# Kernel tuning notes

Measured on AMD Instinct MI355X. Metric: run time of the kernel, lower is better.

## Reference

```python
import jax, jax.numpy as jnp
import numpy as np

B, S, E, H, D, P = 4, 2048, 1024, 16, 64, 64  # batch, seq, embed, heads, head_dim, position_dim
MASKED_BIAS = -10000.0


def setup_inputs() -> dict:
    key = jax.random.key(0)
    ks = jax.random.split(key, 24)
    n = lambda k, sh: jax.random.normal(k, sh, dtype=jnp.float32)
    eyeD = jnp.eye(D, dtype=jnp.float32)
    eyeH = jnp.eye(H, dtype=jnp.float32)
    inp = {
        'hidden_states': n(ks[0], (B, S, E)),
        'position_states': n(ks[1], (B, S, P)),
        # Conv2D per-head projections (identity init + perturbation): [H, D, D]
        'Wq': eyeD[None] + 0.02 * n(ks[2], (H, D, D)), 'bq': 0.01 * n(ks[3], (H, D)),
        'Wk': eyeD[None] + 0.02 * n(ks[4], (H, D, D)), 'bk': 0.01 * n(ks[5], (H, D)),
        'Wv': eyeD[None] + 0.02 * n(ks[6], (H, D, D)), 'bv': 0.01 * n(ks[7], (H, D)),
        # Conv2D(transpose=True) cross-head mix: weight [H_out, H_in, D], bias [H, D]
        'Wqh': eyeH[:, :, None] + 0.02 * n(ks[8], (H, H, D)), 'bqh': 0.01 * n(ks[9], (H, D)),
        'Wkh': eyeH[:, :, None] + 0.02 * n(ks[10], (H, H, D)), 'bkh': 0.01 * n(ks[11], (H, D)),
        'Wvh': eyeH[:, :, None] + 0.02 * n(ks[12], (H, H, D)), 'bvh': 0.01 * n(ks[13], (H, D)),
        # p_attn Conv1D: position_dim -> 3*head_dim
        'Wp': 0.02 * n(ks[14], (P, 3 * D)), 'bp': 0.01 * n(ks[15], (3 * D,)),
        # position_conv expand: weight [3, 1, H], bias [H]
        'Wpe': 0.02 * n(ks[16], (3, 1, H)), 'bpe': 0.01 * n(ks[17], (H,)),
        # c_proj Conv1D: E -> E
        'Wc': 0.02 * n(ks[18], (E, E)), 'bc': 0.01 * n(ks[19], (E,)),
    }
    return inp


def _attention(hidden_states, position_states, Wq, bq, Wqh, bqh, Wk, bk, Wkh, bkh,
               Wv, bv, Wvh, bvh, Wp, bp, Wpe, bpe, Wc, bc):
    b, s, _ = hidden_states.shape
    x = hidden_states.reshape(b, s, H, D)

    def proj(Wa, ba, Wh, bh):
        # Conv2D: per-head linear within head_dim
        y = jnp.einsum('bshd,hde->bshe', x, Wa) + ba
        # Conv2D(transpose): mix across heads, per feature dim d
        return jnp.einsum('bshd,ghd->bsgd', y, Wh) + bh

    q = proj(Wq, bq, Wqh, bqh)  # [b,s,H,D]
    k = proj(Wk, bk, Wkh, bkh)
    v = proj(Wv, bv, Wvh, bvh)

    # p_attn (Conv1D) -> [b,s,3,D]; p_expand broadcasts each var across heads
    p = (position_states @ Wp + bp).reshape(b, s, 3, D)
    pe = p[..., None, :] * Wpe[:, 0, :][:, :, None] + bpe[:, None]  # [b,s,3,H,D]
    q = q + pe[:, :, 0]
    k = k + pe[:, :, 1]
    v = v + pe[:, :, 2]

    q = q.transpose(0, 2, 1, 3)  # [b,H,s,D]
    k = k.transpose(0, 2, 1, 3)
    v = v.transpose(0, 2, 1, 3)

    scores = jnp.einsum('bhqd,bhkd->bhqk', q, k) / jnp.sqrt(jnp.float32(D))
    causal = jnp.tril(jnp.ones((s, s), dtype=bool))
    scores = jnp.where(causal, scores, jnp.float32(MASKED_BIAS))
    w = jax.nn.softmax(scores, axis=-1)
    o = jnp.einsum('bhqk,bhkd->bhqd', w, v)
    o = o.transpose(0, 2, 1, 3).reshape(b, s, E)
    return o @ Wc + bc


def reference(hidden_states, position_states, Wq, bq, Wqh, bqh, Wk, bk, Wkh, bkh,
              Wv, bv, Wvh, bvh, Wp, bp, Wpe, bpe, Wc, bc):
    return _attention(hidden_states, position_states, Wq, bq, Wqh, bqh, Wk, bk,
                      Wkh, bkh, Wv, bv, Wvh, bvh, Wp, bp, Wpe, bpe, Wc, bc)
```

## Files before the change

kernel.cpp:

```cpp
#include <hip/hip_runtime.h>
#include <stdint.h>
#include <stddef.h>

using bf16x8 = __attribute__((ext_vector_type(8))) __bf16;
using f32x4  = __attribute__((ext_vector_type(4))) float;
using u16x8  = __attribute__((ext_vector_type(8))) unsigned short;
using u16x4  = __attribute__((ext_vector_type(4))) unsigned short;
typedef unsigned short u16;

#define DEV __device__ __forceinline__

#define QSCALE 0.18033688011112042f
#define SBIAS 32.0f

DEV u16 f2bf(float f) {
  unsigned u = __float_as_uint(f);
  u += 0x7fffu + ((u >> 16) & 1u);
  return (u16)(u >> 16);
}

DEV void gld_lds16(const u16* g, u16* l) {
  __builtin_amdgcn_global_load_lds(
      (__attribute__((address_space(1))) void*)g,
      (__attribute__((address_space(3))) void*)l, 16, 0, 0);
}

__global__ __launch_bounds__(256) void k_packA(const float* __restrict__ hs,
                                               const float* __restrict__ ps,
                                               u16* __restrict__ A) {
  int idx = blockIdx.x * 256 + threadIdx.x;
  int t  = idx / 272;
  int c4 = (idx - t * 272) * 4;
  float4 f;
  if (c4 < 1024) f = *(const float4*)(hs + (size_t)t * 1024 + c4);
  else           f = *(const float4*)(ps + (size_t)t * 64 + (c4 - 1024));
  u16x4 o4;
  o4[0] = f2bf(f.x); o4[1] = f2bf(f.y); o4[2] = f2bf(f.z); o4[3] = f2bf(f.w);
  *(u16x4*)(A + (size_t)t * 1088 + c4) = o4;
}

__global__ __launch_bounds__(256) void k_buildW(const float* __restrict__ Wq, const float* __restrict__ Wk,
                                                const float* __restrict__ Wv, const float* __restrict__ Wqh,
                                                const float* __restrict__ Wkh, const float* __restrict__ Wvh,
                                                const float* __restrict__ Wp, const float* __restrict__ Wpe,
                                                u16* __restrict__ Wt) {
  int idx = blockIdx.x * 256 + threadIdx.x;
  int n = idx / 1088, kk = idx - n * 1088;
  int which = n >> 10, g = (n >> 6) & 15, e = n & 63;
  const float* Wa = (which == 0) ? Wq : (which == 1) ? Wk : Wv;
  const float* Wh = (which == 0) ? Wqh : (which == 1) ? Wkh : Wvh;
  float val;
  if (kk < 1024) {
    int h = kk >> 6, d = kk & 63;
    val = Wa[(size_t)(h * 64 + d) * 64 + e] * Wh[(size_t)(g * 16 + h) * 64 + e];
  } else {
    int p = kk - 1024;
    val = Wp[(size_t)p * 192 + which * 64 + e] * Wpe[which * 16 + g];
  }
  if (which == 0) val *= QSCALE;
  Wt[idx] = f2bf(val);
}

__global__ __launch_bounds__(256) void k_buildBias(const float* __restrict__ bq, const float* __restrict__ bk,
                                                   const float* __restrict__ bv, const float* __restrict__ Wqh,
                                                   const float* __restrict__ Wkh, const float* __restrict__ Wvh,
                                                   const float* __restrict__ bqh, const float* __restrict__ bkh,
                                                   const float* __restrict__ bvh, const float* __restrict__ bp,
                                                   const float* __restrict__ Wpe, const float* __restrict__ bpe,
                                                   float* __restrict__ bias) {
  int n = blockIdx.x * 256 + threadIdx.x;
  int which = n >> 10, g = (n >> 6) & 15, e = n & 63;
  const float* ba = (which == 0) ? bq : (which == 1) ? bk : bv;
  const float* Wh = (which == 0) ? Wqh : (which == 1) ? Wkh : Wvh;
  const float* bh = (which == 0) ? bqh : (which == 1) ? bkh : bvh;
  float s = bh[g * 64 + e] + bp[which * 64 + e] * Wpe[which * 16 + g] + bpe[g];
  for (int h = 0; h < 16; ++h) s += ba[h * 64 + e] * Wh[(g * 16 + h) * 64 + e];
  if (which == 0) s *= QSCALE;
  bias[n] = s;
}

__global__ __launch_bounds__(256) void k_transWc(const float* __restrict__ Wc, u16* __restrict__ WcT) {
  __shared__ float tile[32][33];
  int tx = threadIdx.x & 31, ty = threadIdx.x >> 5;
  int n0 = blockIdx.x * 32, k0 = blockIdx.y * 32;
#pragma unroll
  for (int i = 0; i < 32; i += 8)
    tile[ty + i][tx] = Wc[(size_t)(k0 + ty + i) * 1024 + n0 + tx];
  __syncthreads();
#pragma unroll
  for (int i = 0; i < 32; i += 8)
    WcT[(size_t)(n0 + ty + i) * 1024 + k0 + tx] = f2bf(tile[tx][ty + i]);
}

template <int EPI>
__global__ __launch_bounds__(256) void gemm128(const u16* __restrict__ A, const u16* __restrict__ Bt,
                                               const float* __restrict__ bias,
                                               u16* __restrict__ qo, u16* __restrict__ ko, u16* __restrict__ vo,
                                               float* __restrict__ outf, int M, int N, int K, int NT) {
  __shared__ alignas(16) u16 As[2][8192];
  __shared__ alignas(16) u16 Bs[2][8192];
  const int tid = threadIdx.x;
  const int l = tid & 63, w = tid >> 6;
  const int lr = l & 15, lg = l >> 4;
  const int wm = w >> 1, wn = w & 1;

  const int nwg = gridDim.x;
  const int cpx = nwg >> 3;
  const int virt = (blockIdx.x & 7) * cpx + (blockIdx.x >> 3);
  const int m0 = (virt / NT) * 128, n0 = (virt - (virt / NT) * NT) * 128;

  const int KT = K >> 6;

  f32x4 acc[4][4] = {};

#pragma unroll
  for (int call = 0; call < 4; ++call) {
    int ci = (call * 4 + w) * 64 + l;
    int row = ci >> 3, s = ci & 7;
    int kq = (s ^ (row & 7)) * 8;
    gld_lds16(A + (size_t)(m0 + row) * K + kq, &As[0][(call * 4 + w) * 512]);
    gld_lds16(Bt + (size_t)(n0 + row) * K + kq, &Bs[0][(call * 4 + w) * 512]);
  }

  int cur = 0;
  for (int kt = 0; kt < KT; ++kt) {
    if (kt + 1 < KT) {
      const int kb = (kt + 1) * 64;
#pragma unroll
      for (int call = 0; call < 4; ++call) {
        int ci = (call * 4 + w) * 64 + l;
        int row = ci >> 3, s = ci & 7;
        int kq = (s ^ (row & 7)) * 8;
        gld_lds16(A + (size_t)(m0 + row) * K + kb + kq, &As[cur ^ 1][(call * 4 + w) * 512]);
        gld_lds16(Bt + (size_t)(n0 + row) * K + kb + kq, &Bs[cur ^ 1][(call * 4 + w) * 512]);
      }
      asm volatile("s_waitcnt vmcnt(8)" ::: "memory");
    } else {
      asm volatile("s_waitcnt vmcnt(0)" ::: "memory");
    }
    __builtin_amdgcn_s_barrier();
    asm volatile("" ::: "memory");

    const u16* AsC = As[cur];
    const u16* BsC = Bs[cur];
#pragma unroll
    for (int kk = 0; kk < 2; ++kk) {
      bf16x8 af[4], bfr[4];
#pragma unroll
      for (int mf = 0; mf < 4; ++mf) {
        int row = wm * 64 + mf * 16 + lr;
        int byo = row * 128 + (((kk * 32 + lg * 8) * 2) ^ ((row & 7) << 4));
        af[mf] = *(const bf16x8*)((const char*)AsC + byo);
      }
#pragma unroll
      for (int nf = 0; nf < 4; ++nf) {
        int row = wn * 64 + nf * 16 + lr;
        int byo = row * 128 + (((kk * 32 + lg * 8) * 2) ^ ((row & 7) << 4));
        bfr[nf] = *(const bf16x8*)((const char*)BsC + byo);
      }
      __builtin_amdgcn_s_setprio(1);
#pragma unroll
      for (int mf = 0; mf < 4; ++mf)
#pragma unroll
        for (int nf = 0; nf < 4; ++nf)
          acc[mf][nf] = __builtin_amdgcn_mfma_f32_16x16x32_bf16(af[mf], bfr[nf], acc[mf][nf], 0, 0, 0);
      __builtin_amdgcn_s_setprio(0);
    }

    asm volatile("s_waitcnt lgkmcnt(0)" ::: "memory");
    __builtin_amdgcn_s_barrier();
    asm volatile("" ::: "memory");
    cur ^= 1;
  }

#pragma unroll
  for (int mf = 0; mf < 4; ++mf)
#pragma unroll
    for (int nf = 0; nf < 4; ++nf)
#pragma unroll
      for (int r = 0; r < 4; ++r) {
        int row = m0 + wm * 64 + mf * 16 + lg * 4 + r;
        int col = n0 + wn * 64 + nf * 16 + lr;
        float val = acc[mf][nf][r] + bias[col];
        if (EPI == 0) {
          int which = col >> 10, g = (col >> 6) & 15, e = col & 63;
          int b = row >> 11, si = row & 2047;
          size_t idx = ((size_t)((b * 16 + g) * 2048 + si)) * 64 + e;
          u16 bvv = f2bf(val);
          if (which == 0) qo[idx] = bvv;
          else if (which == 1) ko[idx] = bvv;
          else vo[idx] = bvv;
        } else {
          outf[(size_t)row * N + col] = val;
        }
      }
}

__global__ __launch_bounds__(256) void k_transV(const u16* __restrict__ v, u16* __restrict__ vT) {
  __shared__ u16 t[64][65];
  int bh = blockIdx.y, s0 = blockIdx.x * 64;
  const u16* src = v + ((size_t)bh * 2048 + s0) * 64;
  u16* dst = vT + (size_t)bh * 64 * 2048 + s0;
  int tid = threadIdx.x;
#pragma unroll
  for (int it = 0; it < 2; ++it) {
    int ci = it * 256 + tid;
    int row = ci >> 3, sl = ci & 7;
    u16x8 val = *(const u16x8*)(src + (size_t)row * 64 + sl * 8);
#pragma unroll
    for (int jj = 0; jj < 8; ++jj) t[row][sl * 8 + jj] = val[jj];
  }
  __syncthreads();
#pragma unroll
  for (int it = 0; it < 2; ++it) {
    int ci = it * 256 + tid;
    int d = ci >> 3, sl = ci & 7;
    u16x8 val;
#pragma unroll
    for (int jj = 0; jj < 8; ++jj) {
      int cp = sl * 8 + jj;
      int tt = (cp & 3) * 16 + (cp >> 2);
      val[jj] = t[tt][d];
    }
    *(u16x8*)(dst + (size_t)d * 2048 + sl * 8) = val;
  }
}

__global__ __launch_bounds__(512) void k_attn(const u16* __restrict__ q, const u16* __restrict__ k,
                                              const u16* __restrict__ vt, u16* __restrict__ o) {
  __shared__ alignas(16) u16 Ks[2][4096];
  __shared__ alignas(16) u16 Vs[2][4096];
  __shared__ alignas(16) u16 Ps[8][16 * 72];

  const int tid = threadIdx.x, l = tid & 63, w = tid >> 6;
  const int lr = l & 15, lg = l >> 4;
  const int i = blockIdx.x;
  const int bh = (i & 7) * 8 + ((i >> 3) & 7);
  const int xb = i >> 6;
  const int b = bh >> 4, h = bh & 15;

  const u16* qp = q + (size_t)bh * 2048 * 64;
  const u16* kp = k + (size_t)bh * 2048 * 64;
  const u16* vp = vt + (size_t)bh * 64 * 2048;

  const int srow = tid >> 3;
  const int skq = ((tid & 7) ^ (srow & 7)) * 8;

  bf16x8 ones;
#pragma unroll
  for (int e = 0; e < 8; ++e) ones[e] = (__bf16)1.0f;

  for (int half = 0; half < 2; ++half) {
    const int tile = half ? (15 - xb) : xb;
    const int qr0 = tile * 128 + w * 16;
    const int jmax = 2 * tile + 1;
    const int jmask = qr0 >> 6;

    bf16x8 qf[2];
#pragma unroll
    for (int kk = 0; kk < 2; ++kk)
      qf[kk] = *(const bf16x8*)(qp + (size_t)(qr0 + lr) * 64 + kk * 32 + lg * 8);

    f32x4 oacc[4] = {};
    f32x4 osum = {};

    gld_lds16(kp + (size_t)srow * 64 + skq, &Ks[0][w * 512]);
    gld_lds16(vp + (size_t)srow * 2048 + skq, &Vs[0][w * 512]);

    int cur = 0;
    for (int j = 0; j <= jmax; ++j) {
      if (j < jmax) {
        const int jn = j + 1;
        gld_lds16(kp + (size_t)(jn * 64 + srow) * 64 + skq, &Ks[cur ^ 1][w * 512]);
        gld_lds16(vp + (size_t)srow * 2048 + jn * 64 + skq, &Vs[cur ^ 1][w * 512]);
        asm volatile("s_waitcnt vmcnt(2)" ::: "memory");
      } else {
        asm volatile("s_waitcnt vmcnt(0)" ::: "memory");
      }
      __builtin_amdgcn_s_barrier();
      asm volatile("" ::: "memory");

      if (j <= jmask) {
        const u16* KsC = Ks[cur];
        const u16* VsC = Vs[cur];

        f32x4 sfr[4];
#pragma unroll
        for (int nf = 0; nf < 4; ++nf)
          sfr[nf] = f32x4{-SBIAS, -SBIAS, -SBIAS, -SBIAS};
#pragma unroll
        for (int kk = 0; kk < 2; ++kk) {
          bf16x8 bk[4];
#pragma unroll
          for (int nf = 0; nf < 4; ++nf) {
            int row = nf * 16 + lr;
            int byo = row * 128 + (((kk * 32 + lg * 8) * 2) ^ ((row & 7) << 4));
            bk[nf] = *(const bf16x8*)((const char*)KsC + byo);
          }
          __builtin_amdgcn_s_setprio(1);
#pragma unroll
          for (int nf = 0; nf < 4; ++nf)
            sfr[nf] = __builtin_amdgcn_mfma_f32_16x16x32_bf16(qf[kk], bk[nf], sfr[nf], 0, 0, 0);
          __builtin_amdgcn_s_setprio(0);
        }

        const bool maskt = (j == jmask);
#pragma unroll
        for (int r = 0; r < 4; ++r) {
          float s0 = sfr[0][r], s1 = sfr[1][r], s2 = sfr[2][r], s3 = sfr[3][r];
          if (maskt) {
            int rowg = qr0 + lg * 4 + r;
            int base = j * 64 + lr;
            if (base      > rowg) s0 = -1e30f;
            if (base + 16 > rowg) s1 = -1e30f;
            if (base + 32 > rowg) s2 = -1e30f;
            if (base + 48 > rowg) s3 = -1e30f;
          }
          float p0 = __builtin_amdgcn_exp2f(s0);
          float p1 = __builtin_amdgcn_exp2f(s1);
          float p2 = __builtin_amdgcn_exp2f(s2);
          float p3 = __builtin_amdgcn_exp2f(s3);
          unsigned w0, w1;
          asm("v_cvt_pk_bf16_f32 %0, %1, %2" : "=v"(w0) : "v"(p0), "v"(p1));
          asm("v_cvt_pk_bf16_f32 %0, %1, %2" : "=v"(w1) : "v"(p2), "v"(p3));
          uint2 pw; pw.x = w0; pw.y = w1;
          *(uint2*)&Ps[w][(lg * 4 + r) * 72 + 4 * lr] = pw;
        }

#pragma unroll
        for (int kk = 0; kk < 2; ++kk) {
          bf16x8 pa = *(const bf16x8*)&Ps[w][lr * 72 + kk * 32 + lg * 8];
          bf16x8 bv[4];
#pragma unroll
          for (int df = 0; df < 4; ++df) {
            int row = df * 16 + lr;
            int byo = row * 128 + (((kk * 32 + lg * 8) * 2) ^ ((row & 7) << 4));
            bv[df] = *(const bf16x8*)((const char*)VsC + byo);
          }
          __builtin_amdgcn_s_setprio(1);
#pragma unroll
          for (int df = 0; df < 4; ++df)
            oacc[df] = __builtin_amdgcn_mfma_f32_16x16x32_bf16(pa, bv[df], oacc[df], 0, 0, 0);
          osum = __builtin_amdgcn_mfma_f32_16x16x32_bf16(pa, ones, osum, 0, 0, 0);
          __builtin_amdgcn_s_setprio(0);
        }
      }

      asm volatile("s_waitcnt lgkmcnt(0)" ::: "memory");
      __builtin_amdgcn_s_barrier();
      asm volatile("" ::: "memory");
      cur ^= 1;
    }

#pragma unroll
    for (int r = 0; r < 4; ++r) {
      float inv = 1.0f / osum[r];
      int rowg = qr0 + lg * 4 + r;
#pragma unroll
      for (int df = 0; df < 4; ++df)
        o[((size_t)(b * 2048 + rowg)) * 1024 + h * 64 + df * 16 + lr] = f2bf(oacc[df][r] * inv);
    }
  }
}

extern "C" void kernel_launch(void* const* d_in, const int* in_sizes, int n_in,
                              void* d_out, int out_size, void* d_ws, size_t ws_size,
                              hipStream_t stream) {
  const float* hs  = (const float*)d_in[0];
  const float* pos = (const float*)d_in[1];
  const float* Wq  = (const float*)d_in[2];  const float* bq  = (const float*)d_in[3];
  const float* Wk  = (const float*)d_in[4];  const float* bk  = (const float*)d_in[5];
  const float* Wv  = (const float*)d_in[6];  const float* bv  = (const float*)d_in[7];
  const float* Wqh = (const float*)d_in[8];  const float* bqh = (const float*)d_in[9];
  const float* Wkh = (const float*)d_in[10]; const float* bkh = (const float*)d_in[11];
  const float* Wvh = (const float*)d_in[12]; const float* bvh = (const float*)d_in[13];
  const float* Wp  = (const float*)d_in[14]; const float* bp  = (const float*)d_in[15];
  const float* Wpe = (const float*)d_in[16]; const float* bpe = (const float*)d_in[17];
  const float* Wc  = (const float*)d_in[18]; const float* bc  = (const float*)d_in[19];
  float* out = (float*)d_out;
  char* ws = (char*)d_ws;

  u16*   Abf   = (u16*)  (ws + 0);
  u16*   WT    = (u16*)  (ws + 17825792);
  float* biasq = (float*)(ws + 24510464);
  u16*   WcT   = (u16*)  (ws + 24522752);
  u16*   qb_   = (u16*)  (ws + 26619904);
  u16*   kb_   = (u16*)  (ws + 43397120);
  u16*   vb_   = (u16*)  (ws + 60174336);
  u16*   vTb   = (u16*)  (ws + 76951552);
  u16*   ob    = Abf;

  k_packA<<<8704, 256, 0, stream>>>(hs, pos, Abf);
  k_buildW<<<13056, 256, 0, stream>>>(Wq, Wk, Wv, Wqh, Wkh, Wvh, Wp, Wpe, WT);
  k_buildBias<<<12, 256, 0, stream>>>(bq, bk, bv, Wqh, Wkh, Wvh, bqh, bkh, bvh, bp, Wpe, bpe, biasq);
  k_transWc<<<dim3(32, 32), 256, 0, stream>>>(Wc, WcT);
  gemm128<0><<<1536, 256, 0, stream>>>(Abf, WT, biasq, qb_, kb_, vb_, nullptr, 8192, 3072, 1088, 24);
  k_transV<<<dim3(32, 64), 256, 0, stream>>>(vb_, vTb);
  k_attn<<<512, 512, 0, stream>>>(qb_, kb_, vTb, ob);
  gemm128<1><<<512, 256, 0, stream>>>(ob, WcT, bc, nullptr, nullptr, nullptr, out, 8192, 1024, 1024, 8);
}
```

Measured before the change: 179.4 us.

## Process 32 query rows per wave in attention with 4-wave blocks

```diff
diff --git a/kernel.cpp b/kernel.cpp
--- a/kernel.cpp
+++ b/kernel.cpp
@@ -226,11 +226,11 @@
   }
 }
 
-__global__ __launch_bounds__(512) void k_attn(const u16* __restrict__ q, const u16* __restrict__ k,
+__global__ __launch_bounds__(256) void k_attn(const u16* __restrict__ q, const u16* __restrict__ k,
                                               const u16* __restrict__ vt, u16* __restrict__ o) {
   __shared__ alignas(16) u16 Ks[2][4096];
   __shared__ alignas(16) u16 Vs[2][4096];
-  __shared__ alignas(16) u16 Ps[8][16 * 72];
+  __shared__ alignas(16) u16 Ps[4][32 * 72];
 
   const int tid = threadIdx.x, l = tid & 63, w = tid >> 6;
   const int lr = l & 15, lg = l >> 4;
@@ -243,37 +243,48 @@
   const u16* kp = k + (size_t)bh * 2048 * 64;
   const u16* vp = vt + (size_t)bh * 64 * 2048;
 
-  const int srow = tid >> 3;
-  const int skq = ((tid & 7) ^ (srow & 7)) * 8;
-
   bf16x8 ones;
 #pragma unroll
   for (int e = 0; e < 8; ++e) ones[e] = (__bf16)1.0f;
 
   for (int half = 0; half < 2; ++half) {
     const int tile = half ? (15 - xb) : xb;
-    const int qr0 = tile * 128 + w * 16;
+    const int qr0 = tile * 128 + w * 32;
     const int jmax = 2 * tile + 1;
-    const int jmask = qr0 >> 6;
-
-    bf16x8 qf[2];
-#pragma unroll
-    for (int kk = 0; kk < 2; ++kk)
-      qf[kk] = *(const bf16x8*)(qp + (size_t)(qr0 + lr) * 64 + kk * 32 + lg * 8);
-
-    f32x4 oacc[4] = {};
-    f32x4 osum = {};
-
-    gld_lds16(kp + (size_t)srow * 64 + skq, &Ks[0][w * 512]);
-    gld_lds16(vp + (size_t)srow * 2048 + skq, &Vs[0][w * 512]);
+    const int jmask = (qr0 + 31) >> 6;
+
+    bf16x8 qf[2][2];
+#pragma unroll
+    for (int mf = 0; mf < 2; ++mf)
+#pragma unroll
+      for (int kk = 0; kk < 2; ++kk)
+        qf[mf][kk] = *(const bf16x8*)(qp + (size_t)(qr0 + mf * 16 + lr) * 64 + kk * 32 + lg * 8);
+
+    f32x4 oacc[2][4] = {};
+    f32x4 osum[2] = {};
+
+#pragma unroll
+    for (int c = 0; c < 2; ++c) {
+      int ci = c * 256 + tid;
+      int row = ci >> 3, s = ci & 7;
+      int kq = (s ^ (row & 7)) * 8;
+      gld_lds16(kp + (size_t)row * 64 + kq, &Ks[0][(c * 4 + w) * 512]);
+      gld_lds16(vp + (size_t)row * 2048 + kq, &Vs[0][(c * 4 + w) * 512]);
+    }
 
     int cur = 0;
     for (int j = 0; j <= jmax; ++j) {
       if (j < jmax) {
         const int jn = j + 1;
-        gld_lds16(kp + (size_t)(jn * 64 + srow) * 64 + skq, &Ks[cur ^ 1][w * 512]);
-        gld_lds16(vp + (size_t)srow * 2048 + jn * 64 + skq, &Vs[cur ^ 1][w * 512]);
-        asm volatile("s_waitcnt vmcnt(2)" ::: "memory");
+#pragma unroll
+        for (int c = 0; c < 2; ++c) {
+          int ci = c * 256 + tid;
+          int row = ci >> 3, s = ci & 7;
+          int kq = (s ^ (row & 7)) * 8;
+          gld_lds16(kp + (size_t)(jn * 64 + row) * 64 + kq, &Ks[cur ^ 1][(c * 4 + w) * 512]);
+          gld_lds16(vp + (size_t)row * 2048 + jn * 64 + kq, &Vs[cur ^ 1][(c * 4 + w) * 512]);
+        }
+        asm volatile("s_waitcnt vmcnt(4)" ::: "memory");
       } else {
         asm volatile("s_waitcnt vmcnt(0)" ::: "memory");
       }
@@ -284,10 +295,12 @@
         const u16* KsC = Ks[cur];
         const u16* VsC = Vs[cur];
 
-        f32x4 sfr[4];
-#pragma unroll
-        for (int nf = 0; nf < 4; ++nf)
-          sfr[nf] = f32x4{-SBIAS, -SBIAS, -SBIAS, -SBIAS};
+        f32x4 sfr[2][4];
+#pragma unroll
+        for (int mf = 0; mf < 2; ++mf)
+#pragma unroll
+          for (int nf = 0; nf < 4; ++nf)
+            sfr[mf][nf] = f32x4{-SBIAS, -SBIAS, -SBIAS, -SBIAS};
 #pragma unroll
         for (int kk = 0; kk < 2; ++kk) {
           bf16x8 bk[4];
@@ -299,37 +312,44 @@
           }
           __builtin_amdgcn_s_setprio(1);
 #pragma unroll
-          for (int nf = 0; nf < 4; ++nf)
-            sfr[nf] = __builtin_amdgcn_mfma_f32_16x16x32_bf16(qf[kk], bk[nf], sfr[nf], 0, 0, 0);
+          for (int mf = 0; mf < 2; ++mf)
+#pragma unroll
+            for (int nf = 0; nf < 4; ++nf)
+              sfr[mf][nf] = __builtin_amdgcn_mfma_f32_16x16x32_bf16(qf[mf][kk], bk[nf], sfr[mf][nf], 0, 0, 0);
           __builtin_amdgcn_s_setprio(0);
         }
 
         const bool maskt = (j == jmask);
 #pragma unroll
-        for (int r = 0; r < 4; ++r) {
-          float s0 = sfr[0][r], s1 = sfr[1][r], s2 = sfr[2][r], s3 = sfr[3][r];
-          if (maskt) {
-            int rowg = qr0 + lg * 4 + r;
-            int base = j * 64 + lr;
-            if (base      > rowg) s0 = -1e30f;
-            if (base + 16 > rowg) s1 = -1e30f;
-            if (base + 32 > rowg) s2 = -1e30f;
-            if (base + 48 > rowg) s3 = -1e30f;
+        for (int mf = 0; mf < 2; ++mf)
+#pragma unroll
+          for (int r = 0; r < 4; ++r) {
+            float s0 = sfr[mf][0][r], s1 = sfr[mf][1][r], s2 = sfr[mf][2][r], s3 = sfr[mf][3][r];
+            if (maskt) {
+              int rowg = qr0 + mf * 16 + lg * 4 + r;
+              int base = j * 64 + lr;
+              if (base      > rowg) s0 = -1e30f;
+              if (base + 16 > rowg) s1 = -1e30f;
+              if (base + 32 > rowg) s2 = -1e30f;
+              if (base + 48 > rowg) s3 = -1e30f;
+            }
+            float p0 = __builtin_amdgcn_exp2f(s0);
+            float p1 = __builtin_amdgcn_exp2f(s1);
+            float p2 = __builtin_amdgcn_exp2f(s2);
+            float p3 = __builtin_amdgcn_exp2f(s3);
+            unsigned w0, w1;
+            asm("v_cvt_pk_bf16_f32 %0, %1, %2" : "=v"(w0) : "v"(p0), "v"(p1));
+            asm("v_cvt_pk_bf16_f32 %0, %1, %2" : "=v"(w1) : "v"(p2), "v"(p3));
+            uint2 pw; pw.x = w0; pw.y = w1;
+            *(uint2*)&Ps[w][(mf * 16 + lg * 4 + r) * 72 + 4 * lr] = pw;
           }
-          float p0 = __builtin_amdgcn_exp2f(s0);
-          float p1 = __builtin_amdgcn_exp2f(s1);
-          float p2 = __builtin_amdgcn_exp2f(s2);
-          float p3 = __builtin_amdgcn_exp2f(s3);
-          unsigned w0, w1;
-          asm("v_cvt_pk_bf16_f32 %0, %1, %2" : "=v"(w0) : "v"(p0), "v"(p1));
-          asm("v_cvt_pk_bf16_f32 %0, %1, %2" : "=v"(w1) : "v"(p2), "v"(p3));
-          uint2 pw; pw.x = w0; pw.y = w1;
-          *(uint2*)&Ps[w][(lg * 4 + r) * 72 + 4 * lr] = pw;
-        }
 
 #pragma unroll
         for (int kk = 0; kk < 2; ++kk) {
-          bf16x8 pa = *(const bf16x8*)&Ps[w][lr * 72 + kk * 32 + lg * 8];
+          bf16x8 pa[2];
+#pragma unroll
+          for (int mf = 0; mf < 2; ++mf)
+            pa[mf] = *(const bf16x8*)&Ps[w][(mf * 16 + lr) * 72 + kk * 32 + lg * 8];
           bf16x8 bv[4];
 #pragma unroll
           for (int df = 0; df < 4; ++df) {
@@ -339,9 +359,13 @@
           }
           __builtin_amdgcn_s_setprio(1);
 #pragma unroll
-          for (int df = 0; df < 4; ++df)
-            oacc[df] = __builtin_amdgcn_mfma_f32_16x16x32_bf16(pa, bv[df], oacc[df], 0, 0, 0);
-          osum = __builtin_amdgcn_mfma_f32_16x16x32_bf16(pa, ones, osum, 0, 0, 0);
+          for (int mf = 0; mf < 2; ++mf)
+#pragma unroll
+            for (int df = 0; df < 4; ++df)
+              oacc[mf][df] = __builtin_amdgcn_mfma_f32_16x16x32_bf16(pa[mf], bv[df], oacc[mf][df], 0, 0, 0);
+#pragma unroll
+          for (int mf = 0; mf < 2; ++mf)
+            osum[mf] = __builtin_amdgcn_mfma_f32_16x16x32_bf16(pa[mf], ones, osum[mf], 0, 0, 0);
           __builtin_amdgcn_s_setprio(0);
         }
       }
@@ -353,13 +377,15 @@
     }
 
 #pragma unroll
-    for (int r = 0; r < 4; ++r) {
-      float inv = 1.0f / osum[r];
-      int rowg = qr0 + lg * 4 + r;
-#pragma unroll
-      for (int df = 0; df < 4; ++df)
-        o[((size_t)(b * 2048 + rowg)) * 1024 + h * 64 + df * 16 + lr] = f2bf(oacc[df][r] * inv);
-    }
+    for (int mf = 0; mf < 2; ++mf)
+#pragma unroll
+      for (int r = 0; r < 4; ++r) {
+        float inv = 1.0f / osum[mf][r];
+        int rowg = qr0 + mf * 16 + lg * 4 + r;
+#pragma unroll
+        for (int df = 0; df < 4; ++df)
+          o[((size_t)(b * 2048 + rowg)) * 1024 + h * 64 + df * 16 + lr] = f2bf(oacc[mf][df][r] * inv);
+      }
   }
 }
 
@@ -396,6 +422,6 @@
   k_transWc<<<dim3(32, 32), 256, 0, stream>>>(Wc, WcT);
   gemm128<0><<<1536, 256, 0, stream>>>(Abf, WT, biasq, qb_, kb_, vb_, nullptr, 8192, 3072, 1088, 24);
   k_transV<<<dim3(32, 64), 256, 0, stream>>>(vb_, vTb);
-  k_attn<<<512, 512, 0, stream>>>(qb_, kb_, vTb, ob);
+  k_attn<<<512, 256, 0, stream>>>(qb_, kb_, vTb, ob);
   gemm128<1><<<512, 256, 0, stream>>>(ob, WcT, bc, nullptr, nullptr, nullptr, out, 8192, 1024, 1024, 8);
 }
```

Result: slower. 188.0 us (+4.8%).
